# Kernel tuning notes

Hardware: AMD Instinct MI355X
Metric: run time of the kernel (lower is better)

## Reference

```python
import jax, jax.numpy as jnp
import numpy as np

D_MODEL = 1024
NUM_HEADS = 16
D_K = D_MODEL // NUM_HEADS


def setup_inputs() -> dict:
    key = jax.random.key(0)
    k1, k2, k3 = jax.random.split(key, 3)
    x = jax.random.normal(k1, (2, 2048, D_MODEL), dtype=jnp.float32)
    # torch Linear(d, 3d): weight shape [3d, d], y = x @ W.T
    W_QKV = jax.random.normal(k2, (3 * D_MODEL, D_MODEL), dtype=jnp.float32) * (1.0 / np.sqrt(D_MODEL))
    W_O = jax.random.normal(k3, (D_MODEL, D_MODEL), dtype=jnp.float32) * (1.0 / np.sqrt(D_MODEL))
    return {"x": x, "W_QKV": W_QKV, "W_O": W_O}


def reference(x, W_QKV, W_O):
    B, T, C = x.shape
    qkv = jnp.einsum('btc,fc->btf', x, W_QKV)  # [B,T,3C]
    q, k, v = jnp.split(qkv, 3, axis=-1)
    def heads(t):
        return t.reshape(B, T, NUM_HEADS, D_K).transpose(0, 2, 1, 3)  # [B,H,T,Dk]
    Q, K, V = heads(q), heads(k), heads(v)
    scores = jnp.einsum('bhqd,bhkd->bhqk', Q, K) / jnp.sqrt(jnp.float32(D_K))
    causal = jnp.tril(jnp.ones((T, T), dtype=bool))
    scores = jnp.where(causal, scores, -jnp.inf)
    attn = jax.nn.softmax(scores, axis=-1)
    out = jnp.einsum('bhqk,bhkd->bhqd', attn, V)
    out = out.transpose(0, 2, 1, 3).reshape(B, T, C)
    return jnp.einsum('btc,oc->bto', out, W_O)
```

## Files before the change

### kernel.cpp

```cpp
#include <hip/hip_runtime.h>
#include <hip/hip_bf16.h>
#include <stdint.h>
#include <stddef.h>


typedef __attribute__((ext_vector_type(8))) __bf16 bf16x8;
typedef __attribute__((ext_vector_type(4))) float  f32x4;

#define AS1(p) ((__attribute__((address_space(1))) void*)(p))
#define AS3(p) ((__attribute__((address_space(3))) void*)(p))

static constexpr int Tq    = 2048;
static constexpr int Cd    = 1024;
static constexpr int Hh    = 16;
static constexpr int Mrows = 2 * Tq;

__global__ __launch_bounds__(256) void cvt_bf16_kernel(const float* __restrict__ in,
                                                       __bf16* __restrict__ out, int n8)
{
    int idx    = blockIdx.x * blockDim.x + threadIdx.x;
    int stride = gridDim.x * blockDim.x;
    for (int i = idx; i < n8; i += stride) {
        f32x4 a = ((const f32x4*)in)[i * 2 + 0];
        f32x4 b = ((const f32x4*)in)[i * 2 + 1];
        bf16x8 o;
#pragma unroll
        for (int j = 0; j < 4; ++j) { o[j] = (__bf16)a[j]; o[4 + j] = (__bf16)b[j]; }
        ((bf16x8*)out)[i] = o;
    }
}

__global__ __launch_bounds__(256) void transpose_v_kernel(const __bf16* __restrict__ qkv,
                                                          __bf16* __restrict__ vT)
{
    __shared__ __bf16 tile[64][65];
    const int t   = threadIdx.x;
    const int r0  = blockIdx.x * 64;
    const int hd0 = blockIdx.y * 64;

    {
        const int rr = t >> 2, c16 = (t & 3) * 16;
        const __bf16* src = qkv + (size_t)(r0 + rr) * 3072 + 2048 + hd0 + c16;
        bf16x8 a = *(const bf16x8*)(src);
        bf16x8 b = *(const bf16x8*)(src + 8);
#pragma unroll
        for (int j = 0; j < 8; ++j) { tile[rr][c16 + j] = a[j]; tile[rr][c16 + 8 + j] = b[j]; }
    }
    __syncthreads();
    {
        const int hd_loc = t >> 2, rg = (t & 3) * 16;
        bf16x8 a, b;
#pragma unroll
        for (int j = 0; j < 8; ++j) { a[j] = tile[rg + j][hd_loc]; b[j] = tile[rg + 8 + j][hd_loc]; }
        __bf16* dst = vT + (size_t)(hd0 + hd_loc) * Mrows + r0 + rg;
        *(bf16x8*)(dst)     = a;
        *(bf16x8*)(dst + 8) = b;
    }
}

template <bool OUT_BF16>
__global__ __launch_bounds__(256) void gemm_bt_kernel(const __bf16* __restrict__ A,
                                                      const __bf16* __restrict__ Bm,
                                                      float* __restrict__ Cf,
                                                      __bf16* __restrict__ Cb,
                                                      int N, int K)
{
    __shared__ __align__(16) __bf16 As[128 * 64];
    __shared__ __align__(16) __bf16 Bs[128 * 64];

    const int tid = threadIdx.x;
    const int l   = tid & 63;
    const int w   = tid >> 6;
    const int wr  = w >> 1, wc = w & 1;
    const int lo  = l & 15, hi = l >> 4;
    const int m0  = blockIdx.x * 128;
    const int n0  = blockIdx.y * 128;

    f32x4 acc[4][4] = {};

    for (int kk = 0; kk < K; kk += 64) {
#pragma unroll
        for (int i = 0; i < 4; ++i) {
            int s   = i * 256 + tid;
            int row = s >> 3;
            int gg  = (s & 7) ^ (row & 7);
            const __bf16* srcA = A  + (size_t)(m0 + row) * K + kk + gg * 8;
            const __bf16* srcB = Bm + (size_t)(n0 + row) * K + kk + gg * 8;
            __builtin_amdgcn_global_load_lds(AS1(srcA), AS3((char*)As + s * 16), 16, 0, 0);
            __builtin_amdgcn_global_load_lds(AS1(srcB), AS3((char*)Bs + s * 16), 16, 0, 0);
        }
        __syncthreads();

#pragma unroll
        for (int ks = 0; ks < 2; ++ks) {
            bf16x8 af[4], bfr[4];
#pragma unroll
            for (int m = 0; m < 4; ++m) {
                int row = wr * 64 + m * 16 + lo;
                int gl  = (ks * 4 + hi) ^ (row & 7);
                af[m] = *(const bf16x8*)((const char*)As + row * 128 + gl * 16);
            }
#pragma unroll
            for (int n = 0; n < 4; ++n) {
                int row = wc * 64 + n * 16 + lo;
                int gl  = (ks * 4 + hi) ^ (row & 7);
                bfr[n] = *(const bf16x8*)((const char*)Bs + row * 128 + gl * 16);
            }
#pragma unroll
            for (int m = 0; m < 4; ++m)
#pragma unroll
                for (int n = 0; n < 4; ++n)
                    acc[m][n] = __builtin_amdgcn_mfma_f32_16x16x32_bf16(af[m], bfr[n], acc[m][n], 0, 0, 0);
        }
        __syncthreads();
    }

#pragma unroll
    for (int m = 0; m < 4; ++m)
#pragma unroll
        for (int n = 0; n < 4; ++n)
#pragma unroll
            for (int r = 0; r < 4; ++r) {
                int row = m0 + wr * 64 + m * 16 + hi * 4 + r;
                int col = n0 + wc * 64 + n * 16 + lo;
                if (OUT_BF16) Cb[(size_t)row * N + col] = (__bf16)acc[m][n][r];
                else          Cf[(size_t)row * N + col] = acc[m][n][r];
            }
}

__global__ __launch_bounds__(256) void attn_kernel(const __bf16* __restrict__ qkv,
                                                   const __bf16* __restrict__ vT,
                                                   __bf16* __restrict__ att)
{
    __shared__ __align__(16) __bf16 Ks[2][64 * 64];
    __shared__ __align__(16) __bf16 Vs[2][64 * 64];
    __shared__ __align__(16) __bf16 Ps[4][16 * 64];

    const int tid = threadIdx.x;
    const int l   = tid & 63;
    const int w   = tid >> 6;
    const int lo  = l & 15, hi = l >> 4;

    const int bid = blockIdx.x;
    const int j   = bid & 15;
    const int h   = (bid >> 4) & 15;
    const int b   = bid >> 8;

    const __bf16* Kbase = qkv + (size_t)b * Tq * 3072 + 1024 + h * 64;
    const __bf16* Vbase = vT  + (size_t)h * 64 * Mrows + b * Tq;

    const int s0 = tid, s1 = 256 + tid;
    const int row_s0 = s0 >> 3, gg_s0 = (s0 & 7) ^ (row_s0 & 7);
    const int row_s1 = s1 >> 3, gg_s1 = (s1 & 7) ^ (row_s1 & 7);

    const int qts[2] = {31 - j, j};

    for (int p = 0; p < 2; ++p) {
        const int qt = qts[p];
        const int q0 = qt * 64;
        const int nt = qt + 1;

        bf16x8 qf[2];
        {
            const __bf16* Qp = qkv + (size_t)(b * Tq + q0 + w * 16 + lo) * 3072 + h * 64 + hi * 8;
#pragma unroll
            for (int s = 0; s < 2; ++s) {
                bf16x8 v = *(const bf16x8*)(Qp + s * 32);
#pragma unroll
                for (int jj = 0; jj < 8; ++jj) v[jj] = (__bf16)((float)v[jj] * 0.125f);
                qf[s] = v;
            }
        }

        f32x4 o[4] = {};
        float mrow[4], lsum[4];
#pragma unroll
        for (int r = 0; r < 4; ++r) { mrow[r] = -1e30f; lsum[r] = 0.f; }

        {
            const __bf16* kp0 = Kbase + (size_t)row_s0 * 3072 + gg_s0 * 8;
            const __bf16* kp1 = Kbase + (size_t)row_s1 * 3072 + gg_s1 * 8;
            const __bf16* vp0 = Vbase + (size_t)row_s0 * Mrows + gg_s0 * 8;
            const __bf16* vp1 = Vbase + (size_t)row_s1 * Mrows + gg_s1 * 8;
            __builtin_amdgcn_global_load_lds(AS1(kp0), AS3((char*)Ks[0] + s0 * 16), 16, 0, 0);
            __builtin_amdgcn_global_load_lds(AS1(kp1), AS3((char*)Ks[0] + s1 * 16), 16, 0, 0);
            __builtin_amdgcn_global_load_lds(AS1(vp0), AS3((char*)Vs[0] + s0 * 16), 16, 0, 0);
            __builtin_amdgcn_global_load_lds(AS1(vp1), AS3((char*)Vs[0] + s1 * 16), 16, 0, 0);
        }
        __syncthreads();

        int cur = 0;
        for (int t = 0; t < nt; ++t) {
            const int k0 = t * 64;

            if (t + 1 < nt) {
                const int kn = k0 + 64;
                const __bf16* kp0 = Kbase + (size_t)(kn + row_s0) * 3072 + gg_s0 * 8;
                const __bf16* kp1 = Kbase + (size_t)(kn + row_s1) * 3072 + gg_s1 * 8;
                const __bf16* vp0 = Vbase + (size_t)row_s0 * Mrows + kn + gg_s0 * 8;
                const __bf16* vp1 = Vbase + (size_t)row_s1 * Mrows + kn + gg_s1 * 8;
                __builtin_amdgcn_global_load_lds(AS1(kp0), AS3((char*)Ks[cur ^ 1] + s0 * 16), 16, 0, 0);
                __builtin_amdgcn_global_load_lds(AS1(kp1), AS3((char*)Ks[cur ^ 1] + s1 * 16), 16, 0, 0);
                __builtin_amdgcn_global_load_lds(AS1(vp0), AS3((char*)Vs[cur ^ 1] + s0 * 16), 16, 0, 0);
                __builtin_amdgcn_global_load_lds(AS1(vp1), AS3((char*)Vs[cur ^ 1] + s1 * 16), 16, 0, 0);
            }

            f32x4 sf[4] = {};
#pragma unroll
            for (int ks = 0; ks < 2; ++ks)
#pragma unroll
                for (int n = 0; n < 4; ++n) {
                    int row = n * 16 + lo;
                    int gl  = (ks * 4 + hi) ^ (row & 7);
                    bf16x8 kf = *(const bf16x8*)((const char*)Ks[cur] + row * 128 + gl * 16);
                    sf[n] = __builtin_amdgcn_mfma_f32_16x16x32_bf16(qf[ks], kf, sf[n], 0, 0, 0);
                }

            const int qg = q0 + w * 16 + hi * 4;
#pragma unroll
            for (int n = 0; n < 4; ++n) {
                int kg = k0 + n * 16 + lo;
#pragma unroll
                for (int r = 0; r < 4; ++r)
                    if (kg > qg + r) sf[n][r] = -1e30f;
            }

#pragma unroll
            for (int r = 0; r < 4; ++r) {
                float mx = fmaxf(fmaxf(sf[0][r], sf[1][r]), fmaxf(sf[2][r], sf[3][r]));
                mx = fmaxf(mx, __shfl_xor(mx, 1));
                mx = fmaxf(mx, __shfl_xor(mx, 2));
                mx = fmaxf(mx, __shfl_xor(mx, 4));
                mx = fmaxf(mx, __shfl_xor(mx, 8));
                float mnew = fmaxf(mrow[r], mx);
                float fac  = __expf(mrow[r] - mnew);
                mrow[r] = mnew;

                float rs = 0.f;
                const int q_loc = hi * 4 + r;
#pragma unroll
                for (int n = 0; n < 4; ++n) {
                    float  pv = __expf(sf[n][r] - mnew);
                    __bf16 pb = (__bf16)pv;
                    rs += (float)pb;
                    int k    = n * 16 + lo;
                    int byte = q_loc * 128 + ((k * 2) ^ ((q_loc & 7) << 4));
                    *(__bf16*)((char*)Ps[w] + byte) = pb;
                }
                rs += __shfl_xor(rs, 1);
                rs += __shfl_xor(rs, 2);
                rs += __shfl_xor(rs, 4);
                rs += __shfl_xor(rs, 8);
                lsum[r] = lsum[r] * fac + rs;
#pragma unroll
                for (int nd = 0; nd < 4; ++nd) o[nd][r] *= fac;
            }

#pragma unroll
            for (int ks = 0; ks < 2; ++ks) {
                int glq = (ks * 4 + hi) ^ (lo & 7);
                bf16x8 pa = *(const bf16x8*)((const char*)Ps[w] + lo * 128 + glq * 16);
#pragma unroll
                for (int nd = 0; nd < 4; ++nd) {
                    int row = nd * 16 + lo;
                    int gl  = (ks * 4 + hi) ^ (row & 7);
                    bf16x8 vb = *(const bf16x8*)((const char*)Vs[cur] + row * 128 + gl * 16);
                    o[nd] = __builtin_amdgcn_mfma_f32_16x16x32_bf16(pa, vb, o[nd], 0, 0, 0);
                }
            }

            __syncthreads();
            cur ^= 1;
        }

#pragma unroll
        for (int nd = 0; nd < 4; ++nd)
#pragma unroll
            for (int r = 0; r < 4; ++r) {
                float val = o[nd][r] / lsum[r];
                int row = b * Tq + q0 + w * 16 + hi * 4 + r;
                int col = h * 64 + nd * 16 + lo;
                att[(size_t)row * Cd + col] = (__bf16)val;
            }
    }
}

extern "C" void kernel_launch(void* const* d_in, const int* in_sizes, int n_in,
                              void* d_out, int out_size, void* d_ws, size_t ws_size,
                              hipStream_t stream)
{
    (void)in_sizes; (void)n_in; (void)out_size; (void)ws_size;

    const float* x    = (const float*)d_in[0];
    const float* Wqkv = (const float*)d_in[1];
    const float* Wo   = (const float*)d_in[2];
    float*       out  = (float*)d_out;

    char* ws = (char*)d_ws;
    __bf16* xb    = (__bf16*)(ws);
    __bf16* wqkvb = (__bf16*)(ws + (size_t)8  * 1024 * 1024);
    __bf16* wob   = (__bf16*)(ws + (size_t)14 * 1024 * 1024);
    __bf16* qkvb  = (__bf16*)(ws + (size_t)16 * 1024 * 1024);
    __bf16* attb  = (__bf16*)(ws + (size_t)40 * 1024 * 1024);
    __bf16* vTb   = xb;

    cvt_bf16_kernel<<<2048, 256, 0, stream>>>(x,    xb,    Mrows * Cd / 8);
    cvt_bf16_kernel<<<1536, 256, 0, stream>>>(Wqkv, wqkvb, 3 * Cd * Cd / 8);
    cvt_bf16_kernel<<<512,  256, 0, stream>>>(Wo,   wob,   Cd * Cd / 8);

    dim3 g1(Mrows / 128, 3 * Cd / 128);
    gemm_bt_kernel<true><<<g1, 256, 0, stream>>>(xb, wqkvb, nullptr, qkvb, 3 * Cd, Cd);

    dim3 gt(Mrows / 64, Cd / 64);
    transpose_v_kernel<<<gt, 256, 0, stream>>>(qkvb, vTb);

    attn_kernel<<<512, 256, 0, stream>>>(qkvb, vTb, attb);

    dim3 g2(Mrows / 128, Cd / 128);
    gemm_bt_kernel<false><<<g2, 256, 0, stream>>>(attb, wob, out, nullptr, Cd, Cd);
}
```

Before: 221.8 us.

## Rework attention to 32x32 MFMA with register-resident P and lazy rescale

```diff
diff --git a/kernel.cpp b/kernel.cpp
--- a/kernel.cpp
+++ b/kernel.cpp
@@ -4,16 +4,19 @@
 #include <stddef.h>
 
 
-typedef __attribute__((ext_vector_type(8))) __bf16 bf16x8;
-typedef __attribute__((ext_vector_type(4))) float  f32x4;
+typedef __attribute__((ext_vector_type(8)))  __bf16   bf16x8;
+typedef __attribute__((ext_vector_type(4)))  float    f32x4;
+typedef __attribute__((ext_vector_type(16))) float    f32x16;
+typedef __attribute__((ext_vector_type(4)))  uint32_t u32x4;
 
 #define AS1(p) ((__attribute__((address_space(1))) void*)(p))
 #define AS3(p) ((__attribute__((address_space(3))) void*)(p))
 
 static constexpr int Tq    = 2048;
 static constexpr int Cd    = 1024;
-static constexpr int Hh    = 16;
 static constexpr int Mrows = 2 * Tq;
+
+#define QSCALE 0.18033688011112042f
 
 __global__ __launch_bounds__(256) void cvt_bf16_kernel(const float* __restrict__ in,
                                                        __bf16* __restrict__ out, int n8)
@@ -63,7 +66,7 @@
                                                       const __bf16* __restrict__ Bm,
                                                       float* __restrict__ Cf,
                                                       __bf16* __restrict__ Cb,
-                                                      int N, int K)
+                                                      int N, int K, int qcols, float qscale)
 {
     __shared__ __align__(16) __bf16 As[128 * 64];
     __shared__ __align__(16) __bf16 Bs[128 * 64];
@@ -123,23 +126,24 @@
             for (int r = 0; r < 4; ++r) {
                 int row = m0 + wr * 64 + m * 16 + hi * 4 + r;
                 int col = n0 + wc * 64 + n * 16 + lo;
-                if (OUT_BF16) Cb[(size_t)row * N + col] = (__bf16)acc[m][n][r];
-                else          Cf[(size_t)row * N + col] = acc[m][n][r];
-            }
-}
-
-__global__ __launch_bounds__(256) void attn_kernel(const __bf16* __restrict__ qkv,
+                float v = acc[m][n][r];
+                if (col < qcols) v *= qscale;
+                if (OUT_BF16) Cb[(size_t)row * N + col] = (__bf16)v;
+                else          Cf[(size_t)row * N + col] = v;
+            }
+}
+
+__global__ __launch_bounds__(128) void attn_kernel(const __bf16* __restrict__ qkv,
                                                    const __bf16* __restrict__ vT,
                                                    __bf16* __restrict__ att)
 {
     __shared__ __align__(16) __bf16 Ks[2][64 * 64];
     __shared__ __align__(16) __bf16 Vs[2][64 * 64];
-    __shared__ __align__(16) __bf16 Ps[4][16 * 64];
 
     const int tid = threadIdx.x;
     const int l   = tid & 63;
     const int w   = tid >> 6;
-    const int lo  = l & 15, hi = l >> 4;
+    const int lo5 = l & 31, hi5 = l >> 5;
 
     const int bid = blockIdx.x;
     const int j   = bid & 15;
@@ -149,43 +153,31 @@
     const __bf16* Kbase = qkv + (size_t)b * Tq * 3072 + 1024 + h * 64;
     const __bf16* Vbase = vT  + (size_t)h * 64 * Mrows + b * Tq;
 
-    const int s0 = tid, s1 = 256 + tid;
-    const int row_s0 = s0 >> 3, gg_s0 = (s0 & 7) ^ (row_s0 & 7);
-    const int row_s1 = s1 >> 3, gg_s1 = (s1 & 7) ^ (row_s1 & 7);
-
     const int qts[2] = {31 - j, j};
 
     for (int p = 0; p < 2; ++p) {
-        const int qt = qts[p];
-        const int q0 = qt * 64;
-        const int nt = qt + 1;
-
-        bf16x8 qf[2];
+        const int qt  = qts[p];
+        const int qb0 = qt * 64;
+        const int nt  = qt + 1;
+
+        bf16x8 qf[4];
         {
-            const __bf16* Qp = qkv + (size_t)(b * Tq + q0 + w * 16 + lo) * 3072 + h * 64 + hi * 8;
-#pragma unroll
-            for (int s = 0; s < 2; ++s) {
-                bf16x8 v = *(const bf16x8*)(Qp + s * 32);
-#pragma unroll
-                for (int jj = 0; jj < 8; ++jj) v[jj] = (__bf16)((float)v[jj] * 0.125f);
-                qf[s] = v;
-            }
-        }
-
-        f32x4 o[4] = {};
-        float mrow[4], lsum[4];
-#pragma unroll
-        for (int r = 0; r < 4; ++r) { mrow[r] = -1e30f; lsum[r] = 0.f; }
-
-        {
-            const __bf16* kp0 = Kbase + (size_t)row_s0 * 3072 + gg_s0 * 8;
-            const __bf16* kp1 = Kbase + (size_t)row_s1 * 3072 + gg_s1 * 8;
-            const __bf16* vp0 = Vbase + (size_t)row_s0 * Mrows + gg_s0 * 8;
-            const __bf16* vp1 = Vbase + (size_t)row_s1 * Mrows + gg_s1 * 8;
-            __builtin_amdgcn_global_load_lds(AS1(kp0), AS3((char*)Ks[0] + s0 * 16), 16, 0, 0);
-            __builtin_amdgcn_global_load_lds(AS1(kp1), AS3((char*)Ks[0] + s1 * 16), 16, 0, 0);
-            __builtin_amdgcn_global_load_lds(AS1(vp0), AS3((char*)Vs[0] + s0 * 16), 16, 0, 0);
-            __builtin_amdgcn_global_load_lds(AS1(vp1), AS3((char*)Vs[0] + s1 * 16), 16, 0, 0);
+            const __bf16* Qp = qkv + (size_t)(b * Tq + qb0 + w * 32 + lo5) * 3072 + h * 64 + hi5 * 8;
+#pragma unroll
+            for (int ds = 0; ds < 4; ++ds) qf[ds] = *(const bf16x8*)(Qp + ds * 16);
+        }
+
+        f32x16 o0 = {}, o1 = {};
+        float m = -1e30f, lsum = 0.f;
+
+#pragma unroll
+        for (int i = 0; i < 4; ++i) {
+            int s = i * 128 + tid;
+            int row = s >> 3, g = (s & 7) ^ (row & 7);
+            __builtin_amdgcn_global_load_lds(AS1(Kbase + (size_t)row * 3072 + g * 8),
+                                             AS3((char*)Ks[0] + s * 16), 16, 0, 0);
+            __builtin_amdgcn_global_load_lds(AS1(Vbase + (size_t)row * Mrows + g * 8),
+                                             AS3((char*)Vs[0] + s * 16), 16, 0, 0);
         }
         __syncthreads();
 
@@ -195,93 +187,138 @@
 
             if (t + 1 < nt) {
                 const int kn = k0 + 64;
-                const __bf16* kp0 = Kbase + (size_t)(kn + row_s0) * 3072 + gg_s0 * 8;
-                const __bf16* kp1 = Kbase + (size_t)(kn + row_s1) * 3072 + gg_s1 * 8;
-                const __bf16* vp0 = Vbase + (size_t)row_s0 * Mrows + kn + gg_s0 * 8;
-                const __bf16* vp1 = Vbase + (size_t)row_s1 * Mrows + kn + gg_s1 * 8;
-                __builtin_amdgcn_global_load_lds(AS1(kp0), AS3((char*)Ks[cur ^ 1] + s0 * 16), 16, 0, 0);
-                __builtin_amdgcn_global_load_lds(AS1(kp1), AS3((char*)Ks[cur ^ 1] + s1 * 16), 16, 0, 0);
-                __builtin_amdgcn_global_load_lds(AS1(vp0), AS3((char*)Vs[cur ^ 1] + s0 * 16), 16, 0, 0);
-                __builtin_amdgcn_global_load_lds(AS1(vp1), AS3((char*)Vs[cur ^ 1] + s1 * 16), 16, 0, 0);
-            }
-
-            f32x4 sf[4] = {};
-#pragma unroll
-            for (int ks = 0; ks < 2; ++ks)
-#pragma unroll
-                for (int n = 0; n < 4; ++n) {
-                    int row = n * 16 + lo;
-                    int gl  = (ks * 4 + hi) ^ (row & 7);
+#pragma unroll
+                for (int i = 0; i < 4; ++i) {
+                    int s = i * 128 + tid;
+                    int row = s >> 3, g = (s & 7) ^ (row & 7);
+                    __builtin_amdgcn_global_load_lds(AS1(Kbase + (size_t)(kn + row) * 3072 + g * 8),
+                                                     AS3((char*)Ks[cur ^ 1] + s * 16), 16, 0, 0);
+                    __builtin_amdgcn_global_load_lds(AS1(Vbase + (size_t)row * Mrows + kn + g * 8),
+                                                     AS3((char*)Vs[cur ^ 1] + s * 16), 16, 0, 0);
+                }
+            }
+
+            f32x16 sf0 = {}, sf1 = {};
+#pragma unroll
+            for (int ds = 0; ds < 4; ++ds) {
+                {
+                    int row = lo5;
+                    int gl  = (ds * 2 + hi5) ^ (row & 7);
                     bf16x8 kf = *(const bf16x8*)((const char*)Ks[cur] + row * 128 + gl * 16);
-                    sf[n] = __builtin_amdgcn_mfma_f32_16x16x32_bf16(qf[ks], kf, sf[n], 0, 0, 0);
-                }
-
-            const int qg = q0 + w * 16 + hi * 4;
-#pragma unroll
-            for (int n = 0; n < 4; ++n) {
-                int kg = k0 + n * 16 + lo;
-#pragma unroll
-                for (int r = 0; r < 4; ++r)
-                    if (kg > qg + r) sf[n][r] = -1e30f;
-            }
-
-#pragma unroll
-            for (int r = 0; r < 4; ++r) {
-                float mx = fmaxf(fmaxf(sf[0][r], sf[1][r]), fmaxf(sf[2][r], sf[3][r]));
-                mx = fmaxf(mx, __shfl_xor(mx, 1));
-                mx = fmaxf(mx, __shfl_xor(mx, 2));
-                mx = fmaxf(mx, __shfl_xor(mx, 4));
-                mx = fmaxf(mx, __shfl_xor(mx, 8));
-                float mnew = fmaxf(mrow[r], mx);
-                float fac  = __expf(mrow[r] - mnew);
-                mrow[r] = mnew;
-
-                float rs = 0.f;
-                const int q_loc = hi * 4 + r;
-#pragma unroll
-                for (int n = 0; n < 4; ++n) {
-                    float  pv = __expf(sf[n][r] - mnew);
-                    __bf16 pb = (__bf16)pv;
-                    rs += (float)pb;
-                    int k    = n * 16 + lo;
-                    int byte = q_loc * 128 + ((k * 2) ^ ((q_loc & 7) << 4));
-                    *(__bf16*)((char*)Ps[w] + byte) = pb;
-                }
-                rs += __shfl_xor(rs, 1);
-                rs += __shfl_xor(rs, 2);
-                rs += __shfl_xor(rs, 4);
-                rs += __shfl_xor(rs, 8);
-                lsum[r] = lsum[r] * fac + rs;
-#pragma unroll
-                for (int nd = 0; nd < 4; ++nd) o[nd][r] *= fac;
-            }
-
-#pragma unroll
-            for (int ks = 0; ks < 2; ++ks) {
-                int glq = (ks * 4 + hi) ^ (lo & 7);
-                bf16x8 pa = *(const bf16x8*)((const char*)Ps[w] + lo * 128 + glq * 16);
-#pragma unroll
-                for (int nd = 0; nd < 4; ++nd) {
-                    int row = nd * 16 + lo;
-                    int gl  = (ks * 4 + hi) ^ (row & 7);
-                    bf16x8 vb = *(const bf16x8*)((const char*)Vs[cur] + row * 128 + gl * 16);
-                    o[nd] = __builtin_amdgcn_mfma_f32_16x16x32_bf16(pa, vb, o[nd], 0, 0, 0);
-                }
-            }
+                    sf0 = __builtin_amdgcn_mfma_f32_32x32x16_bf16(kf, qf[ds], sf0, 0, 0, 0);
+                }
+                {
+                    int row = 32 + lo5;
+                    int gl  = (ds * 2 + hi5) ^ (row & 7);
+                    bf16x8 kf = *(const bf16x8*)((const char*)Ks[cur] + row * 128 + gl * 16);
+                    sf1 = __builtin_amdgcn_mfma_f32_32x32x16_bf16(kf, qf[ds], sf1, 0, 0, 0);
+                }
+            }
+
+            if (t == qt) {
+                const int ql = w * 32 + lo5;
+#pragma unroll
+                for (int r = 0; r < 16; ++r) {
+                    int kc = (r & 3) + 8 * (r >> 2) + 4 * hi5;
+                    if (kc      > ql) sf0[r] = -1e30f;
+                    if (kc + 32 > ql) sf1[r] = -1e30f;
+                }
+            }
+
+            float pmh = fmaxf(sf0[0], sf0[1]);
+#pragma unroll
+            for (int r = 2; r < 16; ++r) pmh = fmaxf(pmh, sf0[r]);
+#pragma unroll
+            for (int r = 0; r < 16; ++r) pmh = fmaxf(pmh, sf1[r]);
+            float pm = fmaxf(pmh, __shfl_xor(pmh, 32));
+
+            if (__any(pm > m + 8.0f)) {
+                float mnew = fmaxf(m, pm);
+                float fac  = exp2f(m - mnew);
+                m = mnew;
+                lsum *= fac;
+#pragma unroll
+                for (int r = 0; r < 16; ++r) {
+                    int qreg = (r & 3) + 8 * (r >> 2) + 4 * hi5;
+                    float fr = __shfl(fac, qreg);
+                    o0[r] *= fr;
+                    o1[r] *= fr;
+                }
+            }
+
+            float psum = 0.f;
+#pragma unroll
+            for (int kb = 0; kb < 2; ++kb) {
+                uint32_t W[8];
+#pragma unroll
+                for (int wd = 0; wd < 8; ++wd) {
+                    float sa = (kb == 0) ? sf0[2 * wd]     : sf1[2 * wd];
+                    float sb = (kb == 0) ? sf0[2 * wd + 1] : sf1[2 * wd + 1];
+                    float pa = exp2f(sa - m);
+                    float pb = exp2f(sb - m);
+                    __bf16 ba = (__bf16)pa, bb = (__bf16)pb;
+                    psum += (float)ba + (float)bb;
+                    W[wd] = (uint32_t)__builtin_bit_cast(uint16_t, ba)
+                          | ((uint32_t)__builtin_bit_cast(uint16_t, bb) << 16);
+                }
+                uint32_t Za = __shfl_xor(hi5 ? W[0] : W[2], 32);
+                uint32_t Zb = __shfl_xor(hi5 ? W[1] : W[3], 32);
+                uint32_t Zc = __shfl_xor(hi5 ? W[4] : W[6], 32);
+                uint32_t Zd = __shfl_xor(hi5 ? W[5] : W[7], 32);
+
+                {
+                    u32x4 fw = { hi5 ? Za : W[0], hi5 ? Zb : W[1],
+                                 hi5 ? W[2] : Za, hi5 ? W[3] : Zb };
+                    bf16x8 pa = __builtin_bit_cast(bf16x8, fw);
+                    const int kstep = kb * 2;
+                    {
+                        int row = lo5;
+                        int gl  = (kstep * 2 + hi5) ^ (row & 7);
+                        bf16x8 vb = *(const bf16x8*)((const char*)Vs[cur] + row * 128 + gl * 16);
+                        o0 = __builtin_amdgcn_mfma_f32_32x32x16_bf16(pa, vb, o0, 0, 0, 0);
+                    }
+                    {
+                        int row = 32 + lo5;
+                        int gl  = (kstep * 2 + hi5) ^ (row & 7);
+                        bf16x8 vb = *(const bf16x8*)((const char*)Vs[cur] + row * 128 + gl * 16);
+                        o1 = __builtin_amdgcn_mfma_f32_32x32x16_bf16(pa, vb, o1, 0, 0, 0);
+                    }
+                }
+                {
+                    u32x4 fw = { hi5 ? Zc : W[4], hi5 ? Zd : W[5],
+                                 hi5 ? W[6] : Zc, hi5 ? W[7] : Zd };
+                    bf16x8 pa = __builtin_bit_cast(bf16x8, fw);
+                    const int kstep = kb * 2 + 1;
+                    {
+                        int row = lo5;
+                        int gl  = (kstep * 2 + hi5) ^ (row & 7);
+                        bf16x8 vb = *(const bf16x8*)((const char*)Vs[cur] + row * 128 + gl * 16);
+                        o0 = __builtin_amdgcn_mfma_f32_32x32x16_bf16(pa, vb, o0, 0, 0, 0);
+                    }
+                    {
+                        int row = 32 + lo5;
+                        int gl  = (kstep * 2 + hi5) ^ (row & 7);
+                        bf16x8 vb = *(const bf16x8*)((const char*)Vs[cur] + row * 128 + gl * 16);
+                        o1 = __builtin_amdgcn_mfma_f32_32x32x16_bf16(pa, vb, o1, 0, 0, 0);
+                    }
+                }
+            }
+            psum += __shfl_xor(psum, 32);
+            lsum += psum;
 
             __syncthreads();
             cur ^= 1;
         }
 
-#pragma unroll
-        for (int nd = 0; nd < 4; ++nd)
-#pragma unroll
-            for (int r = 0; r < 4; ++r) {
-                float val = o[nd][r] / lsum[r];
-                int row = b * Tq + q0 + w * 16 + hi * 4 + r;
-                int col = h * 64 + nd * 16 + lo;
-                att[(size_t)row * Cd + col] = (__bf16)val;
-            }
+        float linv = 1.0f / lsum;
+#pragma unroll
+        for (int r = 0; r < 16; ++r) {
+            int   qreg = (r & 3) + 8 * (r >> 2) + 4 * hi5;
+            float lr   = __shfl(linv, qreg);
+            int   rowg = b * Tq + qb0 + w * 32 + qreg;
+            att[(size_t)rowg * Cd + h * 64 + lo5]      = (__bf16)(o0[r] * lr);
+            att[(size_t)rowg * Cd + h * 64 + 32 + lo5] = (__bf16)(o1[r] * lr);
+        }
     }
 }
 
@@ -309,13 +346,15 @@
     cvt_bf16_kernel<<<512,  256, 0, stream>>>(Wo,   wob,   Cd * Cd / 8);
 
     dim3 g1(Mrows / 128, 3 * Cd / 128);
-    gemm_bt_kernel<true><<<g1, 256, 0, stream>>>(xb, wqkvb, nullptr, qkvb, 3 * Cd, Cd);
+    gemm_bt_kernel<true><<<g1, 256, 0, stream>>>(xb, wqkvb, nullptr, qkvb, 3 * Cd, Cd,
+                                                 1024, QSCALE);
 
     dim3 gt(Mrows / 64, Cd / 64);
     transpose_v_kernel<<<gt, 256, 0, stream>>>(qkvb, vTb);
 
-    attn_kernel<<<512, 256, 0, stream>>>(qkvb, vTb, attb);
+    attn_kernel<<<512, 128, 0, stream>>>(qkvb, vTb, attb);
 
     dim3 g2(Mrows / 128, Cd / 128);
-    gemm_bt_kernel<false><<<g2, 256, 0, stream>>>(attb, wob, out, nullptr, Cd, Cd);
-}
+    gemm_bt_kernel<false><<<g2, 256, 0, stream>>>(attb, wob, out, nullptr, Cd, Cd,
+                                                  0, 1.0f);
+}
```

New measurement: 214.7 us. -3.2%, faster.
